# Performance work log

Hardware: AMD Instinct MI355X
Metric: run time of the kernel (lower is better)

## Reference

```python
import jax, jax.numpy as jnp
import numpy as np

N = 50000      # nodes
E = 600000     # edges (before self-loops)
F_IN = 128     # input features
H = 128        # hidden width
C = 64         # classes
NEG_SLOPE = 0.2


def setup_inputs() -> dict:
    key = jax.random.key(0)
    ks = jax.random.split(key, 16)
    x = jax.random.normal(ks[0], (N, F_IN), dtype=jnp.float32)
    edge_index = jax.random.randint(ks[1], (2, E), 0, N, dtype=jnp.int32)
    dims = [(F_IN, H), (H, H), (H, C)]
    inp = {"x": x, "edge_index": edge_index}
    for l, (din, dout) in enumerate(dims):
        kw, ka, kb = jax.random.split(ks[2 + l], 3)
        scale = 1.0 / np.sqrt(din)
        inp[f"W{l}"] = jax.random.normal(kw, (din, dout), dtype=jnp.float32) * scale
        inp[f"a_src{l}"] = jax.random.normal(ka, (dout,), dtype=jnp.float32) * 0.1
        inp[f"a_dst{l}"] = jax.random.normal(kb, (dout,), dtype=jnp.float32) * 0.1
        inp[f"b{l}"] = jnp.zeros((dout,), dtype=jnp.float32)
    return inp


def gat_conv(x, src, dst, W, a_s, a_d, b):
    n = x.shape[0]
    h = x @ W                                   # [n, dout]
    alpha = jax.nn.leaky_relu((h @ a_s)[src] + (h @ a_d)[dst], NEG_SLOPE)  # [e]
    # segment softmax over destination-node neighborhoods
    m = jax.ops.segment_max(alpha, dst, num_segments=n)
    ex = jnp.exp(alpha - m[dst])
    denom = jax.ops.segment_sum(ex, dst, num_segments=n)
    coef = ex / denom[dst]                      # [e]
    out = jax.ops.segment_sum(h[src] * coef[:, None], dst, num_segments=n)
    return out + b


def reference(x, edge_index, W0, a_src0, a_dst0, b0, W1, a_src1, a_dst1, b1, W2, a_src2, a_dst2, b2):
    n = x.shape[0]
    loops = jnp.arange(n, dtype=edge_index.dtype)   # add_self_loops=True (PyG default)
    src = jnp.concatenate([edge_index[0], loops])
    dst = jnp.concatenate([edge_index[1], loops])
    h = gat_conv(x, src, dst, W0, a_src0, a_dst0, b0)
    h = h * jax.nn.sigmoid(h)                        # SiLU between layers
    h = gat_conv(h, src, dst, W1, a_src1, a_dst1, b1)
    h = h * jax.nn.sigmoid(h)
    h = gat_conv(h, src, dst, W2, a_src2, a_dst2, b2)
    return jax.nn.log_softmax(h, axis=1)
```

## Files before the change

### kernel.cpp

```cpp
#include <hip/hip_runtime.h>
#include <math.h>

#define NEG_SLOPE 0.2f
constexpr int BS_SCAN = 1024;
constexpr int HB_MAX = 160;
constexpr int WPB    = 32;

typedef __attribute__((ext_vector_type(8))) short bfrag;
typedef __attribute__((ext_vector_type(4))) float f32x4;

__device__ __forceinline__ float lrelu(float x) { return x > 0.f ? x : NEG_SLOPE * x; }

__device__ __forceinline__ unsigned short f2bf(float f) {
    union { float f; unsigned u; } v; v.f = f;
    unsigned r = v.u + 0x7fffu + ((v.u >> 16) & 1u);
    return (unsigned short)(r >> 16);
}
__device__ __forceinline__ float bf2f_lo(unsigned p) { union { unsigned u; float f; } v; v.u = p << 16; return v.f; }
__device__ __forceinline__ float bf2f_hi(unsigned p) { union { unsigned u; float f; } v; v.u = p & 0xffff0000u; return v.f; }

__device__ __forceinline__ void wswz_body(const float* __restrict__ W, unsigned short* __restrict__ out,
                                          int DOUT, int tid) {
    int lane = tid & 63;
    int g = tid >> 6;
    int NT = DOUT >> 4;
    int tile = g % NT, kstep = g / NT;
    int q = lane >> 4, c = lane & 15;
    int n_ = tile * 16 + c;
    unsigned short v[8];
#pragma unroll
    for (int j = 0; j < 8; ++j) {
        int k = kstep * 32 + q * 8 + j;
        v[j] = f2bf(W[k * DOUT + n_]);
    }
    uint4 o;
    o.x = (unsigned)v[0] | ((unsigned)v[1] << 16);
    o.y = (unsigned)v[2] | ((unsigned)v[3] << 16);
    o.z = (unsigned)v[4] | ((unsigned)v[5] << 16);
    o.w = (unsigned)v[6] | ((unsigned)v[7] << 16);
    *(uint4*)(out + (size_t)tid * 8) = o;
}

__global__ __launch_bounds__(256) void histswz_kernel(
    const int* __restrict__ dstv, unsigned* __restrict__ hist32, unsigned char* __restrict__ rank8,
    int E, int hb, int nw,
    const float* __restrict__ W0, const float* __restrict__ W1, const float* __restrict__ W2,
    unsigned short* __restrict__ wz0, unsigned short* __restrict__ wz1, unsigned short* __restrict__ wz2)
{
    __shared__ unsigned bins[12544];
    int b = blockIdx.x;
    if (b >= hb) {
        int wb = b - hb;
        if (wb < 8)       wswz_body(W0, wz0, 128, wb * 256 + threadIdx.x);
        else if (wb < 16) wswz_body(W1, wz1, 128, (wb - 8) * 256 + threadIdx.x);
        else {
            int tid = (wb - 16) * 256 + threadIdx.x;
            if (tid < 1024) wswz_body(W2, wz2, 64, tid);
        }
        return;
    }
    int tid = threadIdx.x;
    for (int i = tid; i < nw; i += 256) bins[i] = 0u;
    __syncthreads();
    int base = b * 4096;
#pragma unroll
    for (int j = 0; j < 4; ++j) {
        int e0 = base + j * 1024 + tid * 4;
        if (e0 + 3 < E) {
            int4 d4 = *(const int4*)(dstv + e0);
            unsigned r0, r1, r2, r3;
            { int sh = (d4.x & 3) * 8; r0 = (atomicAdd(&bins[d4.x >> 2], 1u << sh) >> sh) & 0xffu; }
            { int sh = (d4.y & 3) * 8; r1 = (atomicAdd(&bins[d4.y >> 2], 1u << sh) >> sh) & 0xffu; }
            { int sh = (d4.z & 3) * 8; r2 = (atomicAdd(&bins[d4.z >> 2], 1u << sh) >> sh) & 0xffu; }
            { int sh = (d4.w & 3) * 8; r3 = (atomicAdd(&bins[d4.w >> 2], 1u << sh) >> sh) & 0xffu; }
            *(unsigned*)(rank8 + e0) = r0 | (r1 << 8) | (r2 << 16) | (r3 << 24);
        } else {
            for (int k = 0; k < 4; ++k) {
                int e = e0 + k;
                if (e < E) {
                    int d = dstv[e];
                    int sh = (d & 3) * 8;
                    rank8[e] = (unsigned char)((atomicAdd(&bins[d >> 2], 1u << sh) >> sh) & 0xffu);
                }
            }
        }
    }
    __syncthreads();
    unsigned* hrow = hist32 + (size_t)b * nw;
    for (int i = tid; i < nw; i += 256) hrow[i] = bins[i];
}

__global__ __launch_bounds__(1024) void scan1_kernel(const int* __restrict__ counts,
                                                     int* __restrict__ excl,
                                                     int* __restrict__ totals, int n) {
    __shared__ int sm[BS_SCAN];
    int tid = threadIdx.x;
    int i = blockIdx.x * BS_SCAN + tid;
    int v = (i < n) ? counts[i] : 0;
    int val = v;
    sm[tid] = val;
    for (int off = 1; off < BS_SCAN; off <<= 1) {
        __syncthreads();
        int t = (tid >= off) ? sm[tid - off] : 0;
        __syncthreads();
        val += t; sm[tid] = val;
    }
    if (i < n) excl[i] = val - v;
    if (tid == BS_SCAN - 1) totals[blockIdx.x] = val;
}

__global__ __launch_bounds__(1024) void scan23_kernel(int* __restrict__ row_ptr,
                                                      const int* __restrict__ totals,
                                                      int n, int E, int nb) {
    __shared__ int s_off;
    int tid = threadIdx.x;
    if (tid < 64) {
        int v = (tid < blockIdx.x && tid < nb) ? totals[tid] : 0;
#pragma unroll
        for (int off = 32; off; off >>= 1) v += __shfl_xor(v, off);
        if (tid == 0) s_off = v;
    }
    __syncthreads();
    int off = s_off;
    int i = blockIdx.x * BS_SCAN + tid;
    if (i < n) row_ptr[i] += off;
    if (i == 0) row_ptr[n] = E;
}

template<int DOUT, bool ABF>
__device__ __forceinline__ void gemm_body(
    int bid, const void* __restrict__ Xv, const unsigned short* __restrict__ Wswz,
    const float* __restrict__ avs, const float* __restrict__ avd,
    unsigned* __restrict__ Hout, float* __restrict__ as_out, float* __restrict__ ad_out,
    int n, float* __restrict__ smemw)
{
    constexpr int NT = DOUT / 16;
    constexpr int NCH = NT / 4;
    int lane = threadIdx.x & 63;
    int w = threadIdx.x >> 6;
    int q = lane >> 4, c = lane & 15;
    int rowbase = bid * 64 + w * 16;
    int arow = rowbase + c;

    f32x4 acc[NT];
#pragma unroll
    for (int t = 0; t < NT; ++t) acc[t] = (f32x4){0.f, 0.f, 0.f, 0.f};

#pragma unroll
    for (int ks = 0; ks < 4; ++ks) {
        bfrag a = (bfrag)0;
        int k0 = ks * 32 + q * 8;
        if (ABF) {
            if (arow < n) a = *(const bfrag*)((const unsigned short*)Xv + (size_t)arow * 128 + k0);
        } else {
            if (arow < n) {
                const float* xp = (const float*)Xv + (size_t)arow * 128 + k0;
                float4 x0 = *(const float4*)xp, x1 = *(const float4*)(xp + 4);
                a[0] = (short)f2bf(x0.x); a[1] = (short)f2bf(x0.y);
                a[2] = (short)f2bf(x0.z); a[3] = (short)f2bf(x0.w);
                a[4] = (short)f2bf(x1.x); a[5] = (short)f2bf(x1.y);
                a[6] = (short)f2bf(x1.z); a[7] = (short)f2bf(x1.w);
            }
        }
#pragma unroll
        for (int t = 0; t < NT; ++t) {
            bfrag b = *(const bfrag*)(Wswz + ((size_t)(ks * NT + t) * 64 + lane) * 8);
            acc[t] = __builtin_amdgcn_mfma_f32_16x16x32_bf16(a, b, acc[t], 0, 0, 0);
        }
    }

    float* sm = smemw + w * (16 * 68);
    int dr = lane >> 2;
    int c0 = (lane & 3) * 16;
    float s = 0.f, d = 0.f;

#pragma unroll
    for (int ch = 0; ch < NCH; ++ch) {
        if (ch) {
            asm volatile("s_waitcnt lgkmcnt(0)" ::: "memory");
            __builtin_amdgcn_wave_barrier();
        }
#pragma unroll
        for (int t = 0; t < 4; ++t)
#pragma unroll
            for (int r = 0; r < 4; ++r)
                sm[(q * 4 + r) * 68 + t * 16 + c] = acc[ch * 4 + t][r];
        __builtin_amdgcn_wave_barrier();

#pragma unroll
        for (int it = 0; it < 4; ++it) {
            int r = it * 4 + q;
            int grow = rowbase + r;
            float4 v = *(const float4*)(sm + r * 68 + c * 4);
            uint2 o;
            o.x = (unsigned)f2bf(v.x) | ((unsigned)f2bf(v.y) << 16);
            o.y = (unsigned)f2bf(v.z) | ((unsigned)f2bf(v.w) << 16);
            if (grow < n) *(uint2*)(Hout + (size_t)grow * (DOUT / 2) + ch * 32 + c * 2) = o;
        }
#pragma unroll
        for (int j = 0; j < 16; j += 4) {
            float4 hv = *(const float4*)(sm + dr * 68 + c0 + j);
            float4 av = *(const float4*)(avs + ch * 64 + c0 + j);
            float4 dv = *(const float4*)(avd + ch * 64 + c0 + j);
            s += hv.x * av.x + hv.y * av.y + hv.z * av.z + hv.w * av.w;
            d += hv.x * dv.x + hv.y * dv.y + hv.z * dv.z + hv.w * dv.w;
        }
    }

    s += __shfl_down(s, 2); s += __shfl_down(s, 1);
    d += __shfl_down(d, 2); d += __shfl_down(d, 1);
    int grow = rowbase + dr;
    if ((lane & 3) == 0 && grow < n) { as_out[grow] = s; ad_out[grow] = d; }
}

__global__ __launch_bounds__(256) void scangemm0_kernel(
    const unsigned* __restrict__ hist32, unsigned* __restrict__ off32,
    int* __restrict__ counts, int hb, int nw, int sb,
    const float* __restrict__ X, const unsigned short* __restrict__ wz0,
    const float* __restrict__ avs, const float* __restrict__ avd,
    unsigned* __restrict__ Hout, float* __restrict__ as_out, float* __restrict__ ad_out, int n)
{
    __shared__ unsigned smem[HB_MAX * (WPB + 1)];
    int b = blockIdx.x;
    if (b < sb) {
        unsigned (*tile)[WPB + 1] = (unsigned (*)[WPB + 1])smem;
        int tid = threadIdx.x;
        int w0 = b * WPB;
        int wl = tid & 31;
        int w = w0 + wl;
        for (int r = tid >> 5; r < hb; r += 8)
            tile[r][wl] = (w < nw) ? hist32[(size_t)r * nw + w] : 0u;
        __syncthreads();
        if (tid < WPB) {
            unsigned run = 0;
            for (int r = 0; r < hb; ++r) {
                unsigned v = tile[r][tid];
                tile[r][tid] = run;
                run += v;
            }
            int ww = w0 + tid;
            if (ww < nw) {
                int i0 = ww * 4;
                int4 cv;
                cv.x = (int)(run & 0xffu);         cv.y = (int)((run >> 8) & 0xffu);
                cv.z = (int)((run >> 16) & 0xffu); cv.w = (int)((run >> 24) & 0xffu);
                if (i0 + 3 < n) *(int4*)(counts + i0) = cv;
                else {
                    if (i0 < n)     counts[i0]     = cv.x;
                    if (i0 + 1 < n) counts[i0 + 1] = cv.y;
                    if (i0 + 2 < n) counts[i0 + 2] = cv.z;
                    if (i0 + 3 < n) counts[i0 + 3] = cv.w;
                }
            }
        }
        __syncthreads();
        for (int r = tid >> 5; r < hb; r += 8)
            if (w < nw) off32[(size_t)r * nw + w] = tile[r][wl];
        return;
    }
    gemm_body<128, false>(b - sb, X, wz0, avs, avd, Hout, as_out, ad_out, n, (float*)smem);
}

template<int DOUT>
__global__ __launch_bounds__(256) void gemm_kernel(
    const unsigned* __restrict__ Xb, const unsigned short* __restrict__ Wswz,
    const float* __restrict__ avs, const float* __restrict__ avd,
    unsigned* __restrict__ Hout, float* __restrict__ as_out, float* __restrict__ ad_out, int n)
{
    __shared__ float smem[4 * 16 * 68];
    gemm_body<DOUT, true>(blockIdx.x, Xb, Wswz, avs, avd, Hout, as_out, ad_out, n, smem);
}

__global__ __launch_bounds__(256) void scatter_kernel(
    const int* __restrict__ ei, const unsigned char* __restrict__ rank8,
    const unsigned* __restrict__ off32, const int* __restrict__ row_ptr,
    unsigned short* __restrict__ col, int E, int nw)
{
    int e0 = (blockIdx.x * 256 + (int)threadIdx.x) * 4;
    if (e0 + 3 < E) {
        int4 s4 = *(const int4*)(ei + e0);
        int4 d4 = *(const int4*)(ei + E + e0);
        unsigned r4 = *(const unsigned*)(rank8 + e0);
        size_t bb = (size_t)(e0 >> 12) * nw;
        unsigned o0 = (off32[bb + (d4.x >> 2)] >> ((d4.x & 3) * 8)) & 0xffu;
        unsigned o1 = (off32[bb + (d4.y >> 2)] >> ((d4.y & 3) * 8)) & 0xffu;
        unsigned o2 = (off32[bb + (d4.z >> 2)] >> ((d4.z & 3) * 8)) & 0xffu;
        unsigned o3 = (off32[bb + (d4.w >> 2)] >> ((d4.w & 3) * 8)) & 0xffu;
        col[row_ptr[d4.x] + (int)o0 + (int)(r4 & 0xffu)]         = (unsigned short)s4.x;
        col[row_ptr[d4.y] + (int)o1 + (int)((r4 >> 8) & 0xffu)]  = (unsigned short)s4.y;
        col[row_ptr[d4.z] + (int)o2 + (int)((r4 >> 16) & 0xffu)] = (unsigned short)s4.z;
        col[row_ptr[d4.w] + (int)o3 + (int)((r4 >> 24) & 0xffu)] = (unsigned short)s4.w;
    } else {
        for (int k = 0; k < 4; ++k) {
            int e = e0 + k;
            if (e < E) {
                int d = ei[E + e];
                unsigned o = (off32[(size_t)(e >> 12) * nw + (d >> 2)] >> ((d & 3) * 8)) & 0xffu;
                col[row_ptr[d] + (int)o + (int)rank8[e]] = (unsigned short)ei[e];
            }
        }
    }
}

__global__ __launch_bounds__(256) void agg128_kernel(
    const unsigned* __restrict__ Hb, const float* __restrict__ as_v,
    const float* __restrict__ ad_v, const float* __restrict__ bias,
    const int* __restrict__ row_ptr, const unsigned short* __restrict__ col,
    unsigned* __restrict__ outb, int n)
{
    int lane = threadIdx.x & 63;
    int g = lane >> 4, i = lane & 15;
    int node = blockIdx.x * 16 + (threadIdx.x >> 6) * 4 + g;
    if (node >= n) return;
    int beg = row_ptr[node], end = row_ptr[node + 1];
    float adv = ad_v[node];
    float c_self = __expf(fminf(lrelu(as_v[node] + adv), 60.f));

    uint4 hs = *(const uint4*)(Hb + (size_t)node * 64 + i * 4);
    float acc[8];
    acc[0] = c_self * bf2f_lo(hs.x); acc[1] = c_self * bf2f_hi(hs.x);
    acc[2] = c_self * bf2f_lo(hs.y); acc[3] = c_self * bf2f_hi(hs.y);
    acc[4] = c_self * bf2f_lo(hs.z); acc[5] = c_self * bf2f_hi(hs.z);
    acc[6] = c_self * bf2f_lo(hs.w); acc[7] = c_self * bf2f_hi(hs.w);
    float dsum = (i == 0) ? c_self : 0.f;
    int lanebase = g * 16;

    for (int cb = beg; cb < end; cb += 16) {
        int idx = cb + i;
        int sreg = 0; float creg = 0.f;
        if (idx < end) {
            sreg = col[idx];
            creg = __expf(fminf(lrelu(as_v[sreg] + adv), 60.f));
        }
        dsum += creg;
        int cnt = end - cb; if (cnt > 16) cnt = 16;
        for (int k = 0; k < cnt; k += 4) {
            int s0 = __shfl(sreg, lanebase + k);
            int s1 = __shfl(sreg, lanebase + k + 1);
            int s2 = __shfl(sreg, lanebase + k + 2);
            int s3 = __shfl(sreg, lanebase + k + 3);
            float c0 = __shfl(creg, lanebase + k);
            float c1 = __shfl(creg, lanebase + k + 1);
            float c2 = __shfl(creg, lanebase + k + 2);
            float c3 = __shfl(creg, lanebase + k + 3);
            uint4 h0 = *(const uint4*)(Hb + (size_t)s0 * 64 + i * 4);
            uint4 h1 = *(const uint4*)(Hb + (size_t)s1 * 64 + i * 4);
            uint4 h2 = *(const uint4*)(Hb + (size_t)s2 * 64 + i * 4);
            uint4 h3 = *(const uint4*)(Hb + (size_t)s3 * 64 + i * 4);
            acc[0] += c0 * bf2f_lo(h0.x); acc[1] += c0 * bf2f_hi(h0.x);
            acc[2] += c0 * bf2f_lo(h0.y); acc[3] += c0 * bf2f_hi(h0.y);
            acc[4] += c0 * bf2f_lo(h0.z); acc[5] += c0 * bf2f_hi(h0.z);
            acc[6] += c0 * bf2f_lo(h0.w); acc[7] += c0 * bf2f_hi(h0.w);
            acc[0] += c1 * bf2f_lo(h1.x); acc[1] += c1 * bf2f_hi(h1.x);
            acc[2] += c1 * bf2f_lo(h1.y); acc[3] += c1 * bf2f_hi(h1.y);
            acc[4] += c1 * bf2f_lo(h1.z); acc[5] += c1 * bf2f_hi(h1.z);
            acc[6] += c1 * bf2f_lo(h1.w); acc[7] += c1 * bf2f_hi(h1.w);
            acc[0] += c2 * bf2f_lo(h2.x); acc[1] += c2 * bf2f_hi(h2.x);
            acc[2] += c2 * bf2f_lo(h2.y); acc[3] += c2 * bf2f_hi(h2.y);
            acc[4] += c2 * bf2f_lo(h2.z); acc[5] += c2 * bf2f_hi(h2.z);
            acc[6] += c2 * bf2f_lo(h2.w); acc[7] += c2 * bf2f_hi(h2.w);
            acc[0] += c3 * bf2f_lo(h3.x); acc[1] += c3 * bf2f_hi(h3.x);
            acc[2] += c3 * bf2f_lo(h3.y); acc[3] += c3 * bf2f_hi(h3.y);
            acc[4] += c3 * bf2f_lo(h3.z); acc[5] += c3 * bf2f_hi(h3.z);
            acc[6] += c3 * bf2f_lo(h3.w); acc[7] += c3 * bf2f_hi(h3.w);
        }
    }

#pragma unroll
    for (int off = 8; off; off >>= 1) dsum += __shfl_xor(dsum, off);
    float inv = 1.f / dsum;

    float4 b0v = *(const float4*)(bias + i * 8);
    float4 b1v = *(const float4*)(bias + i * 8 + 4);
    float v0 = acc[0] * inv + b0v.x, v1 = acc[1] * inv + b0v.y;
    float v2 = acc[2] * inv + b0v.z, v3 = acc[3] * inv + b0v.w;
    float v4 = acc[4] * inv + b1v.x, v5 = acc[5] * inv + b1v.y;
    float v6 = acc[6] * inv + b1v.z, v7 = acc[7] * inv + b1v.w;
    v0 /= (1.f + __expf(-v0)); v1 /= (1.f + __expf(-v1));
    v2 /= (1.f + __expf(-v2)); v3 /= (1.f + __expf(-v3));
    v4 /= (1.f + __expf(-v4)); v5 /= (1.f + __expf(-v5));
    v6 /= (1.f + __expf(-v6)); v7 /= (1.f + __expf(-v7));
    uint4 o;
    o.x = (unsigned)f2bf(v0) | ((unsigned)f2bf(v1) << 16);
    o.y = (unsigned)f2bf(v2) | ((unsigned)f2bf(v3) << 16);
    o.z = (unsigned)f2bf(v4) | ((unsigned)f2bf(v5) << 16);
    o.w = (unsigned)f2bf(v6) | ((unsigned)f2bf(v7) << 16);
    *(uint4*)(outb + (size_t)node * 64 + i * 4) = o;
}

__global__ __launch_bounds__(256) void agg64_kernel(
    const unsigned* __restrict__ Hb, const float* __restrict__ as_v,
    const float* __restrict__ ad_v, const float* __restrict__ bias,
    const int* __restrict__ row_ptr, const unsigned short* __restrict__ col,
    float* __restrict__ out, int n)
{
    int lane = threadIdx.x & 63;
    int g = lane >> 4, i = lane & 15;
    int node = blockIdx.x * 16 + (threadIdx.x >> 6) * 4 + g;
    if (node >= n) return;
    int beg = row_ptr[node], end = row_ptr[node + 1];
    float adv = ad_v[node];
    float c_self = __expf(fminf(lrelu(as_v[node] + adv), 60.f));

    uint2 hs = *(const uint2*)(Hb + (size_t)node * 32 + i * 2);
    float acc[4];
    acc[0] = c_self * bf2f_lo(hs.x); acc[1] = c_self * bf2f_hi(hs.x);
    acc[2] = c_self * bf2f_lo(hs.y); acc[3] = c_self * bf2f_hi(hs.y);
    float dsum = (i == 0) ? c_self : 0.f;
    int lanebase = g * 16;

    for (int cb = beg; cb < end; cb += 16) {
        int idx = cb + i;
        int sreg = 0; float creg = 0.f;
        if (idx < end) {
            sreg = col[idx];
            creg = __expf(fminf(lrelu(as_v[sreg] + adv), 60.f));
        }
        dsum += creg;
        int cnt = end - cb; if (cnt > 16) cnt = 16;
        for (int k = 0; k < cnt; k += 4) {
            int s0 = __shfl(sreg, lanebase + k);
            int s1 = __shfl(sreg, lanebase + k + 1);
            int s2 = __shfl(sreg, lanebase + k + 2);
            int s3 = __shfl(sreg, lanebase + k + 3);
            float c0 = __shfl(creg, lanebase + k);
            float c1 = __shfl(creg, lanebase + k + 1);
            float c2 = __shfl(creg, lanebase + k + 2);
            float c3 = __shfl(creg, lanebase + k + 3);
            uint2 h0 = *(const uint2*)(Hb + (size_t)s0 * 32 + i * 2);
            uint2 h1 = *(const uint2*)(Hb + (size_t)s1 * 32 + i * 2);
            uint2 h2 = *(const uint2*)(Hb + (size_t)s2 * 32 + i * 2);
            uint2 h3 = *(const uint2*)(Hb + (size_t)s3 * 32 + i * 2);
            acc[0] += c0 * bf2f_lo(h0.x); acc[1] += c0 * bf2f_hi(h0.x);
            acc[2] += c0 * bf2f_lo(h0.y); acc[3] += c0 * bf2f_hi(h0.y);
            acc[0] += c1 * bf2f_lo(h1.x); acc[1] += c1 * bf2f_hi(h1.x);
            acc[2] += c1 * bf2f_lo(h1.y); acc[3] += c1 * bf2f_hi(h1.y);
            acc[0] += c2 * bf2f_lo(h2.x); acc[1] += c2 * bf2f_hi(h2.x);
            acc[2] += c2 * bf2f_lo(h2.y); acc[3] += c2 * bf2f_hi(h2.y);
            acc[0] += c3 * bf2f_lo(h3.x); acc[1] += c3 * bf2f_hi(h3.x);
            acc[2] += c3 * bf2f_lo(h3.y); acc[3] += c3 * bf2f_hi(h3.y);
        }
    }

#pragma unroll
    for (int off = 8; off; off >>= 1) dsum += __shfl_xor(dsum, off);
    float inv = 1.f / dsum;

    float4 bv = *(const float4*)(bias + i * 4);
    float v0 = acc[0] * inv + bv.x, v1 = acc[1] * inv + bv.y;
    float v2 = acc[2] * inv + bv.z, v3 = acc[3] * inv + bv.w;
    float mx = fmaxf(fmaxf(v0, v1), fmaxf(v2, v3));
#pragma unroll
    for (int off = 8; off; off >>= 1) mx = fmaxf(mx, __shfl_xor(mx, off));
    float sum = __expf(v0 - mx) + __expf(v1 - mx) + __expf(v2 - mx) + __expf(v3 - mx);
#pragma unroll
    for (int off = 8; off; off >>= 1) sum += __shfl_xor(sum, off);
    float ls = mx + logf(sum);
    float4 o = make_float4(v0 - ls, v1 - ls, v2 - ls, v3 - ls);
    *(float4*)(out + (size_t)node * 64 + i * 4) = o;
}

extern "C" void kernel_launch(void* const* d_in, const int* in_sizes, int n_in,
                              void* d_out, int out_size, void* d_ws, size_t ws_size,
                              hipStream_t stream) {
    const float* x   = (const float*)d_in[0];
    const int*   ei  = (const int*)d_in[1];
    const float* W0  = (const float*)d_in[2];
    const float* as0 = (const float*)d_in[3];
    const float* ad0 = (const float*)d_in[4];
    const float* b0  = (const float*)d_in[5];
    const float* W1  = (const float*)d_in[6];
    const float* as1 = (const float*)d_in[7];
    const float* ad1 = (const float*)d_in[8];
    const float* b1  = (const float*)d_in[9];
    const float* W2  = (const float*)d_in[10];
    const float* as2 = (const float*)d_in[11];
    const float* ad2 = (const float*)d_in[12];
    const float* b2  = (const float*)d_in[13];

    int n = in_sizes[0] / 128;
    int E = in_sizes[1] / 2;
    const int* dstv = ei + E;

    int hb = (E + 4095) >> 12;
    int nw = (n + 3) >> 2;

    char* wsp = (char*)d_ws;
    auto alloc = [&](size_t bytes) {
        char* p = wsp;
        wsp += (bytes + 255) & ~(size_t)255;
        return p;
    };
    int*   counts  = (int*)alloc((size_t)n * 4);
    int*   row_ptr = (int*)alloc((size_t)(n + 1) * 4);
    int*   totals  = (int*)alloc(256 * 4);
    unsigned* hist32 = (unsigned*)alloc((size_t)hb * nw * 4);
    unsigned* off32  = (unsigned*)alloc((size_t)hb * nw * 4);
    unsigned char* rank8 = (unsigned char*)alloc((size_t)E);
    unsigned short* col = (unsigned short*)alloc((size_t)E * 2);
    unsigned short* wz0 = (unsigned short*)alloc(128 * 128 * 2);
    unsigned short* wz1 = (unsigned short*)alloc(128 * 128 * 2);
    unsigned short* wz2 = (unsigned short*)alloc(128 * 64 * 2);
    unsigned* hb0  = (unsigned*)alloc((size_t)n * 64 * 4);
    unsigned* hb1  = (unsigned*)alloc((size_t)n * 64 * 4);
    unsigned* hf   = (unsigned*)alloc((size_t)n * 32 * 4);
    unsigned* xb   = (unsigned*)alloc((size_t)n * 64 * 4);
    float*    asbA = (float*)alloc((size_t)n * 4);
    float*    adbA = (float*)alloc((size_t)n * 4);
    float*    asbB = (float*)alloc((size_t)n * 4);
    float*    adbB = (float*)alloc((size_t)n * 4);

    int gemmb = (n + 63) / 64;
    int nodeb = (n + 15) / 16;
    int nb  = (n + BS_SCAN - 1) / BS_SCAN;
    int sb  = (nw + WPB - 1) / WPB;
    int scb = (E + 1023) / 1024;

    histswz_kernel<<<hb + 20, 256, 0, stream>>>(dstv, hist32, rank8, E, hb, nw,
                                                W0, W1, W2, wz0, wz1, wz2);
    scangemm0_kernel<<<sb + gemmb, 256, 0, stream>>>(hist32, off32, counts, hb, nw, sb,
                                                     x, wz0, as0, ad0, hb0, asbA, adbA, n);
    scan1_kernel<<<nb, BS_SCAN, 0, stream>>>(counts, row_ptr, totals, n);
    scan23_kernel<<<nb, BS_SCAN, 0, stream>>>(row_ptr, totals, n, E, nb);
    scatter_kernel<<<scb, 256, 0, stream>>>(ei, rank8, off32, row_ptr, col, E, nw);
    agg128_kernel<<<nodeb, 256, 0, stream>>>(hb0, asbA, adbA, b0, row_ptr, col, xb, n);
    gemm_kernel<128><<<gemmb, 256, 0, stream>>>(xb, wz1, as1, ad1, hb1, asbB, adbB, n);
    agg128_kernel<<<nodeb, 256, 0, stream>>>(hb1, asbB, adbB, b1, row_ptr, col, xb, n);
    gemm_kernel<64><<<gemmb, 256, 0, stream>>>(xb, wz2, as2, ad2, hf, asbA, adbA, n);
    agg64_kernel<<<nodeb, 256, 0, stream>>>(hf, asbA, adbA, b2, row_ptr, col, (float*)d_out, n);
}
```

Before: 227.6 us.

## Merge scan kernels via grid-wide spin counter and widen aggregation unroll

Fuses the two scan passes into one kernel that publishes per-block totals and spins on a global counter (reset in the histogram kernel) before adding prefix offsets, removing one launch. Also vectorises histogram bin zeroing and copy-out with uint4, makes scatter handle two 1024-edge chunks per block, and unrolls the neighbor gather loops in both aggregation kernels from 4 to 8 loads in flight. The spin wait assumes all 49 scan blocks are co-resident. The wider unroll raises register pressure, and when cnt is not a multiple of 8 the loop reads lanes past the valid chunk, relying on zero coefficients there as before.

```diff
diff --git a/kernel.cpp b/kernel.cpp
--- a/kernel.cpp
+++ b/kernel.cpp
@@ -43,7 +43,7 @@
 
 __global__ __launch_bounds__(256) void histswz_kernel(
     const int* __restrict__ dstv, unsigned* __restrict__ hist32, unsigned char* __restrict__ rank8,
-    int E, int hb, int nw,
+    int E, int hb, int nw, int* __restrict__ done,
     const float* __restrict__ W0, const float* __restrict__ W1, const float* __restrict__ W2,
     unsigned short* __restrict__ wz0, unsigned short* __restrict__ wz1, unsigned short* __restrict__ wz2)
 {
@@ -51,6 +51,7 @@
     int b = blockIdx.x;
     if (b >= hb) {
         int wb = b - hb;
+        if (wb == 0 && threadIdx.x == 0) *done = 0;
         if (wb < 8)       wswz_body(W0, wz0, 128, wb * 256 + threadIdx.x);
         else if (wb < 16) wswz_body(W1, wz1, 128, (wb - 8) * 256 + threadIdx.x);
         else {
@@ -60,7 +61,15 @@
         return;
     }
     int tid = threadIdx.x;
-    for (int i = tid; i < nw; i += 256) bins[i] = 0u;
+    int nw4 = nw >> 2;
+    bool v4ok = (nw & 3) == 0;
+    if (v4ok) {
+        uint4 z4; z4.x = z4.y = z4.z = z4.w = 0u;
+        uint4* b4 = (uint4*)bins;
+        for (int i = tid; i < nw4; i += 256) b4[i] = z4;
+    } else {
+        for (int i = tid; i < nw; i += 256) bins[i] = 0u;
+    }
     __syncthreads();
     int base = b * 4096;
 #pragma unroll
@@ -87,13 +96,21 @@
     }
     __syncthreads();
     unsigned* hrow = hist32 + (size_t)b * nw;
-    for (int i = tid; i < nw; i += 256) hrow[i] = bins[i];
-}
-
-__global__ __launch_bounds__(1024) void scan1_kernel(const int* __restrict__ counts,
-                                                     int* __restrict__ excl,
-                                                     int* __restrict__ totals, int n) {
+    if (v4ok) {
+        uint4* h4 = (uint4*)hrow;
+        const uint4* s4 = (const uint4*)bins;
+        for (int i = tid; i < nw4; i += 256) h4[i] = s4[i];
+    } else {
+        for (int i = tid; i < nw; i += 256) hrow[i] = bins[i];
+    }
+}
+
+__global__ __launch_bounds__(1024) void scan_kernel(
+    const int* __restrict__ counts, int* __restrict__ row_ptr,
+    int* __restrict__ totals, int* __restrict__ done, int n, int E, int nb)
+{
     __shared__ int sm[BS_SCAN];
+    __shared__ int s_off;
     int tid = threadIdx.x;
     int i = blockIdx.x * BS_SCAN + tid;
     int v = (i < n) ? counts[i] : 0;
@@ -105,25 +122,21 @@
         __syncthreads();
         val += t; sm[tid] = val;
     }
-    if (i < n) excl[i] = val - v;
-    if (tid == BS_SCAN - 1) totals[blockIdx.x] = val;
-}
-
-__global__ __launch_bounds__(1024) void scan23_kernel(int* __restrict__ row_ptr,
-                                                      const int* __restrict__ totals,
-                                                      int n, int E, int nb) {
-    __shared__ int s_off;
-    int tid = threadIdx.x;
+    if (tid == BS_SCAN - 1) {
+        totals[blockIdx.x] = val;
+        __threadfence();
+        atomicAdd(done, 1);
+    }
     if (tid < 64) {
-        int v = (tid < blockIdx.x && tid < nb) ? totals[tid] : 0;
-#pragma unroll
-        for (int off = 32; off; off >>= 1) v += __shfl_xor(v, off);
-        if (tid == 0) s_off = v;
+        while (atomicAdd(done, 0) < nb) {}
+        __threadfence();
+        int t = (tid < blockIdx.x && tid < nb) ? totals[tid] : 0;
+#pragma unroll
+        for (int off = 32; off; off >>= 1) t += __shfl_xor(t, off);
+        if (tid == 0) s_off = t;
     }
     __syncthreads();
-    int off = s_off;
-    int i = blockIdx.x * BS_SCAN + tid;
-    if (i < n) row_ptr[i] += off;
+    if (i < n) row_ptr[i] = val - v + s_off;
     if (i == 0) row_ptr[n] = E;
 }
 
@@ -276,27 +289,31 @@
     const unsigned* __restrict__ off32, const int* __restrict__ row_ptr,
     unsigned short* __restrict__ col, int E, int nw)
 {
-    int e0 = (blockIdx.x * 256 + (int)threadIdx.x) * 4;
-    if (e0 + 3 < E) {
-        int4 s4 = *(const int4*)(ei + e0);
-        int4 d4 = *(const int4*)(ei + E + e0);
-        unsigned r4 = *(const unsigned*)(rank8 + e0);
-        size_t bb = (size_t)(e0 >> 12) * nw;
-        unsigned o0 = (off32[bb + (d4.x >> 2)] >> ((d4.x & 3) * 8)) & 0xffu;
-        unsigned o1 = (off32[bb + (d4.y >> 2)] >> ((d4.y & 3) * 8)) & 0xffu;
-        unsigned o2 = (off32[bb + (d4.z >> 2)] >> ((d4.z & 3) * 8)) & 0xffu;
-        unsigned o3 = (off32[bb + (d4.w >> 2)] >> ((d4.w & 3) * 8)) & 0xffu;
-        col[row_ptr[d4.x] + (int)o0 + (int)(r4 & 0xffu)]         = (unsigned short)s4.x;
-        col[row_ptr[d4.y] + (int)o1 + (int)((r4 >> 8) & 0xffu)]  = (unsigned short)s4.y;
-        col[row_ptr[d4.z] + (int)o2 + (int)((r4 >> 16) & 0xffu)] = (unsigned short)s4.z;
-        col[row_ptr[d4.w] + (int)o3 + (int)((r4 >> 24) & 0xffu)] = (unsigned short)s4.w;
-    } else {
-        for (int k = 0; k < 4; ++k) {
-            int e = e0 + k;
-            if (e < E) {
-                int d = ei[E + e];
-                unsigned o = (off32[(size_t)(e >> 12) * nw + (d >> 2)] >> ((d & 3) * 8)) & 0xffu;
-                col[row_ptr[d] + (int)o + (int)rank8[e]] = (unsigned short)ei[e];
+    int e0base = blockIdx.x * 2048 + (int)threadIdx.x * 4;
+#pragma unroll
+    for (int j = 0; j < 2; ++j) {
+        int e0 = e0base + j * 1024;
+        if (e0 + 3 < E) {
+            int4 s4 = *(const int4*)(ei + e0);
+            int4 d4 = *(const int4*)(ei + E + e0);
+            unsigned r4 = *(const unsigned*)(rank8 + e0);
+            size_t bb = (size_t)(e0 >> 12) * nw;
+            unsigned o0 = (off32[bb + (d4.x >> 2)] >> ((d4.x & 3) * 8)) & 0xffu;
+            unsigned o1 = (off32[bb + (d4.y >> 2)] >> ((d4.y & 3) * 8)) & 0xffu;
+            unsigned o2 = (off32[bb + (d4.z >> 2)] >> ((d4.z & 3) * 8)) & 0xffu;
+            unsigned o3 = (off32[bb + (d4.w >> 2)] >> ((d4.w & 3) * 8)) & 0xffu;
+            col[row_ptr[d4.x] + (int)o0 + (int)(r4 & 0xffu)]         = (unsigned short)s4.x;
+            col[row_ptr[d4.y] + (int)o1 + (int)((r4 >> 8) & 0xffu)]  = (unsigned short)s4.y;
+            col[row_ptr[d4.z] + (int)o2 + (int)((r4 >> 16) & 0xffu)] = (unsigned short)s4.z;
+            col[row_ptr[d4.w] + (int)o3 + (int)((r4 >> 24) & 0xffu)] = (unsigned short)s4.w;
+        } else {
+            for (int k = 0; k < 4; ++k) {
+                int e = e0 + k;
+                if (e < E) {
+                    int d = ei[E + e];
+                    unsigned o = (off32[(size_t)(e >> 12) * nw + (d >> 2)] >> ((d & 3) * 8)) & 0xffu;
+                    col[row_ptr[d] + (int)o + (int)rank8[e]] = (unsigned short)ei[e];
+                }
             }
         }
     }
@@ -334,19 +351,24 @@
         }
         dsum += creg;
         int cnt = end - cb; if (cnt > 16) cnt = 16;
-        for (int k = 0; k < cnt; k += 4) {
-            int s0 = __shfl(sreg, lanebase + k);
-            int s1 = __shfl(sreg, lanebase + k + 1);
-            int s2 = __shfl(sreg, lanebase + k + 2);
-            int s3 = __shfl(sreg, lanebase + k + 3);
-            float c0 = __shfl(creg, lanebase + k);
-            float c1 = __shfl(creg, lanebase + k + 1);
-            float c2 = __shfl(creg, lanebase + k + 2);
-            float c3 = __shfl(creg, lanebase + k + 3);
+        for (int k = 0; k < cnt; k += 8) {
+            int kb = lanebase + k;
+            int s0 = __shfl(sreg, kb);     int s1 = __shfl(sreg, kb + 1);
+            int s2 = __shfl(sreg, kb + 2); int s3 = __shfl(sreg, kb + 3);
+            int s4 = __shfl(sreg, kb + 4); int s5 = __shfl(sreg, kb + 5);
+            int s6 = __shfl(sreg, kb + 6); int s7 = __shfl(sreg, kb + 7);
+            float c0 = __shfl(creg, kb);     float c1 = __shfl(creg, kb + 1);
+            float c2 = __shfl(creg, kb + 2); float c3 = __shfl(creg, kb + 3);
+            float c4 = __shfl(creg, kb + 4); float c5 = __shfl(creg, kb + 5);
+            float c6 = __shfl(creg, kb + 6); float c7 = __shfl(creg, kb + 7);
             uint4 h0 = *(const uint4*)(Hb + (size_t)s0 * 64 + i * 4);
             uint4 h1 = *(const uint4*)(Hb + (size_t)s1 * 64 + i * 4);
             uint4 h2 = *(const uint4*)(Hb + (size_t)s2 * 64 + i * 4);
             uint4 h3 = *(const uint4*)(Hb + (size_t)s3 * 64 + i * 4);
+            uint4 h4 = *(const uint4*)(Hb + (size_t)s4 * 64 + i * 4);
+            uint4 h5 = *(const uint4*)(Hb + (size_t)s5 * 64 + i * 4);
+            uint4 h6 = *(const uint4*)(Hb + (size_t)s6 * 64 + i * 4);
+            uint4 h7 = *(const uint4*)(Hb + (size_t)s7 * 64 + i * 4);
             acc[0] += c0 * bf2f_lo(h0.x); acc[1] += c0 * bf2f_hi(h0.x);
             acc[2] += c0 * bf2f_lo(h0.y); acc[3] += c0 * bf2f_hi(h0.y);
             acc[4] += c0 * bf2f_lo(h0.z); acc[5] += c0 * bf2f_hi(h0.z);
@@ -363,6 +385,22 @@
             acc[2] += c3 * bf2f_lo(h3.y); acc[3] += c3 * bf2f_hi(h3.y);
             acc[4] += c3 * bf2f_lo(h3.z); acc[5] += c3 * bf2f_hi(h3.z);
             acc[6] += c3 * bf2f_lo(h3.w); acc[7] += c3 * bf2f_hi(h3.w);
+            acc[0] += c4 * bf2f_lo(h4.x); acc[1] += c4 * bf2f_hi(h4.x);
+            acc[2] += c4 * bf2f_lo(h4.y); acc[3] += c4 * bf2f_hi(h4.y);
+            acc[4] += c4 * bf2f_lo(h4.z); acc[5] += c4 * bf2f_hi(h4.z);
+            acc[6] += c4 * bf2f_lo(h4.w); acc[7] += c4 * bf2f_hi(h4.w);
+            acc[0] += c5 * bf2f_lo(h5.x); acc[1] += c5 * bf2f_hi(h5.x);
+            acc[2] += c5 * bf2f_lo(h5.y); acc[3] += c5 * bf2f_hi(h5.y);
+            acc[4] += c5 * bf2f_lo(h5.z); acc[5] += c5 * bf2f_hi(h5.z);
+            acc[6] += c5 * bf2f_lo(h5.w); acc[7] += c5 * bf2f_hi(h5.w);
+            acc[0] += c6 * bf2f_lo(h6.x); acc[1] += c6 * bf2f_hi(h6.x);
+            acc[2] += c6 * bf2f_lo(h6.y); acc[3] += c6 * bf2f_hi(h6.y);
+            acc[4] += c6 * bf2f_lo(h6.z); acc[5] += c6 * bf2f_hi(h6.z);
+            acc[6] += c6 * bf2f_lo(h6.w); acc[7] += c6 * bf2f_hi(h6.w);
+            acc[0] += c7 * bf2f_lo(h7.x); acc[1] += c7 * bf2f_hi(h7.x);
+            acc[2] += c7 * bf2f_lo(h7.y); acc[3] += c7 * bf2f_hi(h7.y);
+            acc[4] += c7 * bf2f_lo(h7.z); acc[5] += c7 * bf2f_hi(h7.z);
+            acc[6] += c7 * bf2f_lo(h7.w); acc[7] += c7 * bf2f_hi(h7.w);
         }
     }
 
@@ -418,19 +456,24 @@
         }
         dsum += creg;
         int cnt = end - cb; if (cnt > 16) cnt = 16;
-        for (int k = 0; k < cnt; k += 4) {
-            int s0 = __shfl(sreg, lanebase + k);
-            int s1 = __shfl(sreg, lanebase + k + 1);
-            int s2 = __shfl(sreg, lanebase + k + 2);
-            int s3 = __shfl(sreg, lanebase + k + 3);
-            float c0 = __shfl(creg, lanebase + k);
-            float c1 = __shfl(creg, lanebase + k + 1);
-            float c2 = __shfl(creg, lanebase + k + 2);
-            float c3 = __shfl(creg, lanebase + k + 3);
+        for (int k = 0; k < cnt; k += 8) {
+            int kb = lanebase + k;
+            int s0 = __shfl(sreg, kb);     int s1 = __shfl(sreg, kb + 1);
+            int s2 = __shfl(sreg, kb + 2); int s3 = __shfl(sreg, kb + 3);
+            int s4 = __shfl(sreg, kb + 4); int s5 = __shfl(sreg, kb + 5);
+            int s6 = __shfl(sreg, kb + 6); int s7 = __shfl(sreg, kb + 7);
+            float c0 = __shfl(creg, kb);     float c1 = __shfl(creg, kb + 1);
+            float c2 = __shfl(creg, kb + 2); float c3 = __shfl(creg, kb + 3);
+            float c4 = __shfl(creg, kb + 4); float c5 = __shfl(creg, kb + 5);
+            float c6 = __shfl(creg, kb + 6); float c7 = __shfl(creg, kb + 7);
             uint2 h0 = *(const uint2*)(Hb + (size_t)s0 * 32 + i * 2);
             uint2 h1 = *(const uint2*)(Hb + (size_t)s1 * 32 + i * 2);
             uint2 h2 = *(const uint2*)(Hb + (size_t)s2 * 32 + i * 2);
             uint2 h3 = *(const uint2*)(Hb + (size_t)s3 * 32 + i * 2);
+            uint2 h4 = *(const uint2*)(Hb + (size_t)s4 * 32 + i * 2);
+            uint2 h5 = *(const uint2*)(Hb + (size_t)s5 * 32 + i * 2);
+            uint2 h6 = *(const uint2*)(Hb + (size_t)s6 * 32 + i * 2);
+            uint2 h7 = *(const uint2*)(Hb + (size_t)s7 * 32 + i * 2);
             acc[0] += c0 * bf2f_lo(h0.x); acc[1] += c0 * bf2f_hi(h0.x);
             acc[2] += c0 * bf2f_lo(h0.y); acc[3] += c0 * bf2f_hi(h0.y);
             acc[0] += c1 * bf2f_lo(h1.x); acc[1] += c1 * bf2f_hi(h1.x);
@@ -439,6 +482,14 @@
             acc[2] += c2 * bf2f_lo(h2.y); acc[3] += c2 * bf2f_hi(h2.y);
             acc[0] += c3 * bf2f_lo(h3.x); acc[1] += c3 * bf2f_hi(h3.x);
             acc[2] += c3 * bf2f_lo(h3.y); acc[3] += c3 * bf2f_hi(h3.y);
+            acc[0] += c4 * bf2f_lo(h4.x); acc[1] += c4 * bf2f_hi(h4.x);
+            acc[2] += c4 * bf2f_lo(h4.y); acc[3] += c4 * bf2f_hi(h4.y);
+            acc[0] += c5 * bf2f_lo(h5.x); acc[1] += c5 * bf2f_hi(h5.x);
+            acc[2] += c5 * bf2f_lo(h5.y); acc[3] += c5 * bf2f_hi(h5.y);
+            acc[0] += c6 * bf2f_lo(h6.x); acc[1] += c6 * bf2f_hi(h6.x);
+            acc[2] += c6 * bf2f_lo(h6.y); acc[3] += c6 * bf2f_hi(h6.y);
+            acc[0] += c7 * bf2f_lo(h7.x); acc[1] += c7 * bf2f_hi(h7.x);
+            acc[2] += c7 * bf2f_lo(h7.y); acc[3] += c7 * bf2f_hi(h7.y);
         }
     }
 
@@ -494,6 +545,7 @@
     int*   counts  = (int*)alloc((size_t)n * 4);
     int*   row_ptr = (int*)alloc((size_t)(n + 1) * 4);
     int*   totals  = (int*)alloc(256 * 4);
+    int*   done    = (int*)alloc(256);
     unsigned* hist32 = (unsigned*)alloc((size_t)hb * nw * 4);
     unsigned* off32  = (unsigned*)alloc((size_t)hb * nw * 4);
     unsigned char* rank8 = (unsigned char*)alloc((size_t)E);
@@ -514,14 +566,13 @@
     int nodeb = (n + 15) / 16;
     int nb  = (n + BS_SCAN - 1) / BS_SCAN;
     int sb  = (nw + WPB - 1) / WPB;
-    int scb = (E + 1023) / 1024;
-
-    histswz_kernel<<<hb + 20, 256, 0, stream>>>(dstv, hist32, rank8, E, hb, nw,
+    int scb = (E + 2047) / 2048;
+
+    histswz_kernel<<<hb + 20, 256, 0, stream>>>(dstv, hist32, rank8, E, hb, nw, done,
                                                 W0, W1, W2, wz0, wz1, wz2);
     scangemm0_kernel<<<sb + gemmb, 256, 0, stream>>>(hist32, off32, counts, hb, nw, sb,
                                                      x, wz0, as0, ad0, hb0, asbA, adbA, n);
-    scan1_kernel<<<nb, BS_SCAN, 0, stream>>>(counts, row_ptr, totals, n);
-    scan23_kernel<<<nb, BS_SCAN, 0, stream>>>(row_ptr, totals, n, E, nb);
+    scan_kernel<<<nb, BS_SCAN, 0, stream>>>(counts, row_ptr, totals, done, n, E, nb);
     scatter_kernel<<<scb, 256, 0, stream>>>(ei, rank8, off32, row_ptr, col, E, nw);
     agg128_kernel<<<nodeb, 256, 0, stream>>>(hb0, asbA, adbA, b0, row_ptr, col, xb, n);
     gemm_kernel<128><<<gemmb, 256, 0, stream>>>(xb, wz1, as1, ad1, hb1, asbB, adbB, n);
```

Result: no change. 228.5 us (+0.4%).
